# Kernel optimization log

Measured on AMD Instinct MI355X. Metric: run time of the kernel, lower is better.

Reference implementation:

```python
import jax, jax.numpy as jnp
import numpy as np

DIM, PATCHES, HID, NCLS, NBLK, PS = 384, 196, 1536, 1000, 24, 16

def fq(w, bits=8):
    # symmetric per-tensor fake quantization (dequantized), as in QAT DynamicQLinear
    n = float(2 ** (bits - 1) - 1)
    s = jnp.max(jnp.abs(w)) / n + 1e-8
    q = jnp.clip(jnp.round(w / s), -n - 1.0, n) * s
    return q

def setup_inputs() -> dict:
    key = jax.random.key(0)
    ks = jax.random.split(key, 12)
    d = {}
    d["x"] = jax.random.normal(ks[0], (64, 3, 224, 224), jnp.float32)
    d["conv_w"] = jax.random.normal(ks[1], (DIM, 3, PS, PS), jnp.float32) * 0.02
    d["conv_b"] = jnp.zeros((DIM,), jnp.float32)
    d["norm1_a"] = jnp.ones((NBLK, DIM), jnp.float32)
    d["norm1_b"] = jnp.zeros((NBLK, DIM), jnp.float32)
    d["attn_w"] = jax.random.normal(ks[2], (NBLK, PATCHES, PATCHES), jnp.float32) * 0.02
    d["attn_b"] = jnp.zeros((NBLK, PATCHES), jnp.float32)
    d["gamma1"] = jnp.full((NBLK, DIM), 1e-4, jnp.float32)
    d["norm2_a"] = jnp.ones((NBLK, DIM), jnp.float32)
    d["norm2_b"] = jnp.zeros((NBLK, DIM), jnp.float32)
    d["mlp_w1"] = jax.random.normal(ks[3], (NBLK, HID, DIM), jnp.float32) * 0.02
    d["mlp_b1"] = jnp.zeros((NBLK, HID), jnp.float32)
    d["mlp_w2"] = jax.random.normal(ks[4], (NBLK, DIM, HID), jnp.float32) * 0.02
    d["mlp_b2"] = jnp.zeros((NBLK, DIM), jnp.float32)
    d["gamma2"] = jnp.full((NBLK, DIM), 1e-4, jnp.float32)
    d["norm_a"] = jnp.ones((DIM,), jnp.float32)
    d["norm_b"] = jnp.zeros((DIM,), jnp.float32)
    d["head_w"] = jax.random.normal(ks[5], (NCLS, DIM), jnp.float32) * 0.02
    d["head_b"] = jnp.zeros((NCLS,), jnp.float32)
    return d

def reference(x, conv_w, conv_b, norm1_a, norm1_b, attn_w, attn_b, gamma1,
              norm2_a, norm2_b, mlp_w1, mlp_b1, mlp_w2, mlp_b2, gamma2,
              norm_a, norm_b, head_w, head_b):
    B = x.shape[0]
    # patch embed: quantized 16x16 stride-16 conv, then flatten(2).transpose(1,2)
    h = jax.lax.conv_general_dilated(x, fq(conv_w), (PS, PS), 'VALID',
                                     dimension_numbers=('NCHW', 'OIHW', 'NCHW'))
    h = h + conv_b[None, :, None, None]
    h = h.reshape(B, DIM, PATCHES).transpose(0, 2, 1)  # [B, 196, 384]

    def step(xc, p):
        a1, b1, aw, ab, g1, a2, b2, w1, bb1, w2, bb2, g2 = p
        # affine norm1 (per-channel)
        t = xc * a1 + b1
        # cross-patch linear applied on transposed layout: out[b,q,d] = sum_p t[b,p,d] W[q,p]
        t = jnp.einsum('bpd,qp->bqd', t, fq(aw)) + ab[None, :, None]
        xc = g1 * t + xc
        # affine norm2 + MLP (384 -> 1536 -> 384, exact GELU)
        t = xc * a2 + b2
        t = jax.nn.gelu(jnp.einsum('bpd,hd->bph', t, fq(w1)) + bb1, approximate=False)
        t = jnp.einsum('bph,dh->bpd', t, fq(w2)) + bb2
        xc = g2 * t + xc
        return xc, None

    h, _ = jax.lax.scan(step, h, (norm1_a, norm1_b, attn_w, attn_b, gamma1,
                                  norm2_a, norm2_b, mlp_w1, mlp_b1, mlp_w2, mlp_b2, gamma2))
    h = h * norm_a + norm_b          # final affine norm
    h = h.mean(axis=1)               # mean pool over patches -> [B, 384]
    return h @ fq(head_w).T + head_b  # [B, 1000]
```

## Files before the change

kernel.cpp:

```cpp
#include <hip/hip_runtime.h>

#define DIM 384
#define PATCHES 196
#define HID 1536
#define NBLK 24
#define NPAD 256
#define XROWS (64 * PATCHES)
#define BDCOLS (64 * DIM)
#define XELEMS (XROWS * DIM)
#define ESTRIDE 132

typedef __attribute__((ext_vector_type(8))) short s8v;
typedef __attribute__((ext_vector_type(4))) float f4v;
typedef unsigned char uchar;
typedef long long i64t;

__device__ __forceinline__ short f2bf(float f) {
  unsigned u = __float_as_uint(f);
  u += 0x7FFFu + ((u >> 16) & 1u);
  return (short)(u >> 16);
}

__device__ __forceinline__ float gelu_f(float x) {
  float u2 = 1.5957691216f * (x + 0.044715f * x * x * x);
  return x / (1.0f + __expf(-u2));
}

__device__ __forceinline__ unsigned pk4_fp8(float a, float b, float c, float d) {
  int lo = __builtin_amdgcn_cvt_pk_fp8_f32(a, b, 0, false);
  int full = __builtin_amdgcn_cvt_pk_fp8_f32(c, d, lo, true);
  return (unsigned)full;
}
__device__ __forceinline__ uchar fp8_1(float a) {
  return (uchar)(__builtin_amdgcn_cvt_pk_fp8_f32(a, a, 0, false) & 0xff);
}

__device__ __forceinline__ void gload_lds16(const void* g, void* l) {
  __builtin_amdgcn_global_load_lds((const __attribute__((address_space(1))) void*)g,
                                   (__attribute__((address_space(3))) void*)l, 16, 0, 0);
}

__global__ __launch_bounds__(256)
void absmax_v4(const float* __restrict__ src, int f4per, int blocks_per,
               unsigned* __restrict__ out) {
  int tens = blockIdx.x / blocks_per;
  int sl = blockIdx.x - tens * blocks_per;
  const float4* p = (const float4*)(src + (size_t)tens * f4per * 4);
  float m = 0.f;
  for (int i = sl * 256 + threadIdx.x; i < f4per; i += blocks_per * 256) {
    float4 v = p[i];
    m = fmaxf(m, fmaxf(fmaxf(fabsf(v.x), fabsf(v.y)), fmaxf(fabsf(v.z), fabsf(v.w))));
  }
  __shared__ float red[256];
  red[threadIdx.x] = m;
  __syncthreads();
  for (int s = 128; s > 0; s >>= 1) {
    if ((int)threadIdx.x < s) red[threadIdx.x] = fmaxf(red[threadIdx.x], red[threadIdx.x + s]);
    __syncthreads();
  }
  if (threadIdx.x == 0) atomicMax(out + tens, __float_as_uint(red[0]));
}

__global__ __launch_bounds__(256)
void quant_w(const float* __restrict__ w, short* __restrict__ q,
             const unsigned* __restrict__ sc, int per, int total) {
  int i = blockIdx.x * 256 + threadIdx.x;
  if (i >= total) return;
  int tens = i / per;
  float s = __uint_as_float(sc[tens]) / 127.0f + 1e-8f;
  float v = rintf(w[i] / s);
  v = fminf(fmaxf(v, -128.0f), 127.0f) * s;
  q[i] = f2bf(v);
}

__global__ __launch_bounds__(256)
void quant_fp8(const float* __restrict__ w, unsigned* __restrict__ q,
               const unsigned* __restrict__ sc, int per, int total4) {
  int i = blockIdx.x * 256 + threadIdx.x;
  if (i >= total4) return;
  int e = i << 2;
  int tens = e / per;
  float s = __uint_as_float(sc[tens]) / 127.0f + 1e-8f;
  float4 w4 = *(const float4*)(w + e);
  float a = fminf(fmaxf(rintf(w4.x / s), -128.0f), 127.0f) * s;
  float b = fminf(fmaxf(rintf(w4.y / s), -128.0f), 127.0f) * s;
  float c = fminf(fmaxf(rintf(w4.z / s), -128.0f), 127.0f) * s;
  float d = fminf(fmaxf(rintf(w4.w / s), -128.0f), 127.0f) * s;
  q[i] = pk4_fp8(a, b, c, d);
}

__global__ __launch_bounds__(256)
void quant_attn_fp8(const float* __restrict__ w, unsigned* __restrict__ q,
                    const unsigned* __restrict__ sc) {
  int i = blockIdx.x * 256 + threadIdx.x;
  if (i >= NBLK * PATCHES * NPAD / 4) return;
  int e = i << 2;
  int col = e & (NPAD - 1);
  int rt = e >> 8;
  int row = rt % PATCHES;
  int tens = rt / PATCHES;
  float s = __uint_as_float(sc[tens]) / 127.0f + 1e-8f;
  const float* wr = w + (size_t)tens * PATCHES * PATCHES + (size_t)row * PATCHES;
  float v[4];
#pragma unroll
  for (int k = 0; k < 4; ++k) {
    int c = col + k;
    v[k] = (c < PATCHES) ? fminf(fmaxf(rintf(wr[c] / s), -128.0f), 127.0f) * s : 0.f;
  }
  q[i] = pk4_fp8(v[0], v[1], v[2], v[3]);
}

__global__ __launch_bounds__(256)
void quant_head_v4(const float* __restrict__ w, float* __restrict__ q,
                   const unsigned* __restrict__ sc) {
  int i = blockIdx.x * 256 + threadIdx.x;
  if (i >= 1000 * DIM / 4) return;
  float s = __uint_as_float(sc[0]) / 127.0f + 1e-8f;
  float4 w4 = *(const float4*)(w + (i << 2));
  float4 o;
  o.x = fminf(fmaxf(rintf(w4.x / s), -128.0f), 127.0f) * s;
  o.y = fminf(fmaxf(rintf(w4.y / s), -128.0f), 127.0f) * s;
  o.z = fminf(fmaxf(rintf(w4.z / s), -128.0f), 127.0f) * s;
  o.w = fminf(fmaxf(rintf(w4.w / s), -128.0f), 127.0f) * s;
  *(float4*)(q + (i << 2)) = o;
}

__global__ __launch_bounds__(256)
void im2col_k(const float* __restrict__ x, short* __restrict__ Xa) {
  int idx = blockIdx.x * 256 + threadIdx.x;
  if (idx >= XROWS * 768 / 4) return;
  int e = idx << 2;
  int r = e / 768, k = e - r * 768;
  int b = r / PATCHES, p = r - b * PATCHES;
  int c = k >> 8, rem = k & 255, ii = rem >> 4, j = rem & 15;
  int ph = p / 14, pw = p - ph * 14;
  const float4 v = *(const float4*)(x + (b * 3 + c) * 50176 + (ph * 16 + ii) * 224 + pw * 16 + j);
  short2* o = (short2*)(Xa + e);
  o[0] = make_short2(f2bf(v.x), f2bf(v.y));
  o[1] = make_short2(f2bf(v.z), f2bf(v.w));
}

__global__ __launch_bounds__(256)
void gemm_conv(const short* __restrict__ A, const short* __restrict__ B,
               float* __restrict__ Xres, const float* __restrict__ bias,
               const float* __restrict__ n1a, const float* __restrict__ n1b,
               uchar* __restrict__ Yt) {
  constexpr int TILE_SHORTS = 192 * 64;
  __shared__ char smem[2 * TILE_SHORTS * 2];
  short* buf0 = (short*)smem;
  float* S = (float*)smem;
  const int lda = 768, K = 768;

  const int t = threadIdx.x;
  const int lane = t & 63;
  const int wid = t >> 6;
  const int wr = wid >> 1, wc = wid & 1;

  const int gx = gridDim.x;
  const int nwg = gx * gridDim.y;
  const int orig = blockIdx.y * gx + blockIdx.x;
  const int q = nwg >> 3, rm = nwg & 7;
  const int xc = orig & 7, jj = orig >> 3;
  const int wg = (xc < rm ? xc * (q + 1) : rm * (q + 1) + (xc - rm) * q) + jj;
  const int bx = wg % gx, by = wg / gx;
  const int m0 = by * 64, n0 = bx * 128;

  f4v acc[2][4];
#pragma unroll
  for (int m = 0; m < 2; ++m)
#pragma unroll
    for (int n = 0; n < 4; ++n) acc[m][n] = (f4v){0.f, 0.f, 0.f, 0.f};

  const int srow = t >> 3;
  const int scol = ((t & 7) ^ (srow & 7)) << 3;
  const short* ga[2];
#pragma unroll
  for (int h = 0; h < 2; ++h) ga[h] = A + (size_t)(m0 + h * 32 + srow) * lda + scol;
  const short* gb[4];
#pragma unroll
  for (int j = 0; j < 4; ++j) gb[j] = B + (size_t)(n0 + j * 32 + srow) * lda + scol;
  short* ldst = buf0 + (t & ~63) * 8;

  auto stage = [&](int slot, int kt) {
    const int koff = kt << 6;
    const int boff = slot * TILE_SHORTS;
    gload_lds16(ga[0] + koff, ldst + boff);
    gload_lds16(ga[1] + koff, ldst + boff + 2048);
#pragma unroll
    for (int j = 0; j < 4; ++j)
      gload_lds16(gb[j] + koff, ldst + boff + 4096 + j * 2048);
  };

  const int l15 = lane & 15, lk = lane >> 4, l7 = lane & 7;
  int paoff[2], pboff[2];
#pragma unroll
  for (int ks = 0; ks < 2; ++ks) {
    const int cgx = ((ks << 2) + lk) ^ l7;
    paoff[ks] = (wr * 32 + l15) * 64 + (cgx << 3);
    pboff[ks] = 4096 + (wc * 64 + l15) * 64 + (cgx << 3);
  }

  const int nk = K >> 6;
  stage(0, 0);
  asm volatile("s_waitcnt vmcnt(0)" ::: "memory");
  __builtin_amdgcn_s_barrier();
  for (int kt = 0; kt < nk; ++kt) {
    const int cur = kt & 1;
    if (kt + 1 < nk) stage(cur ^ 1, kt + 1);
    const short* base = buf0 + cur * TILE_SHORTS;
    s8v af[2][2], bfr[4][2];
#pragma unroll
    for (int m = 0; m < 2; ++m)
#pragma unroll
      for (int ks = 0; ks < 2; ++ks) af[m][ks] = *(const s8v*)(base + paoff[ks] + m * 1024);
#pragma unroll
    for (int n = 0; n < 4; ++n)
#pragma unroll
      for (int ks = 0; ks < 2; ++ks) bfr[n][ks] = *(const s8v*)(base + pboff[ks] + n * 1024);
    asm volatile("s_waitcnt lgkmcnt(0)" ::: "memory");
    __builtin_amdgcn_sched_barrier(0);
    __builtin_amdgcn_s_setprio(1);
#pragma unroll
    for (int m = 0; m < 2; ++m)
#pragma unroll
      for (int n = 0; n < 4; ++n)
#pragma unroll
        for (int ks = 0; ks < 2; ++ks)
          acc[m][n] = __builtin_amdgcn_mfma_f32_16x16x32_bf16(af[m][ks], bfr[n][ks], acc[m][n], 0, 0, 0);
    __builtin_amdgcn_s_setprio(0);
    if (kt + 1 < nk) {
      asm volatile("s_waitcnt vmcnt(0)" ::: "memory");
      __builtin_amdgcn_s_barrier();
    }
  }

  const int cb = (wc << 6) + l15;
  const int rl = t >> 3;
  const int c0 = (t & 7) << 4;
#pragma unroll
  for (int m = 0; m < 2; ++m) {
    __syncthreads();
#pragma unroll
    for (int n = 0; n < 4; ++n) {
      int c = cb + n * 16;
#pragma unroll
      for (int j = 0; j < 4; ++j)
        S[((wr << 4) + (lk << 2) + j) * ESTRIDE + c] = acc[m][n][j];
    }
    __syncthreads();
    const int r = m0 + (rl >> 4) * 32 + m * 16 + (rl & 15);
    const int colg = n0 + c0;
    float xn[16];
#pragma unroll
    for (int i = 0; i < 4; ++i) {
      float4 q4 = *(const float4*)(S + rl * ESTRIDE + c0 + i * 4);
      float4 b4 = *(const float4*)(bias + colg + i * 4);
      float4 o4 = make_float4(q4.x + b4.x, q4.y + b4.y, q4.z + b4.z, q4.w + b4.w);
      *(float4*)(Xres + (size_t)r * DIM + colg + i * 4) = o4;
      xn[4 * i] = o4.x; xn[4 * i + 1] = o4.y; xn[4 * i + 2] = o4.z; xn[4 * i + 3] = o4.w;
    }
    int bb = r / PATCHES, p = r - bb * PATCHES;
    uchar* yrow = Yt + ((size_t)(bb * DIM + colg)) * NPAD + p;
#pragma unroll
    for (int i = 0; i < 4; ++i) {
      float4 a4 = *(const float4*)(n1a + colg + i * 4);
      float4 b4 = *(const float4*)(n1b + colg + i * 4);
      yrow[(4 * i + 0) * NPAD] = fp8_1(xn[4 * i] * a4.x + b4.x);
      yrow[(4 * i + 1) * NPAD] = fp8_1(xn[4 * i + 1] * a4.y + b4.y);
      yrow[(4 * i + 2) * NPAD] = fp8_1(xn[4 * i + 2] * a4.z + b4.z);
      yrow[(4 * i + 3) * NPAD] = fp8_1(xn[4 * i + 3] * a4.w + b4.w);
    }
  }
}

template <int EPI>
__global__ __launch_bounds__(256)
void gemm8(const uchar* __restrict__ A, int lda8, int Mlim,
           const uchar* __restrict__ B, int ldb8, int K,
           float* __restrict__ Xres, uchar* __restrict__ OutB8,
           const float* __restrict__ bias, const float* __restrict__ gamma,
           const float* __restrict__ n2a, const float* __restrict__ n2b,
           const float* __restrict__ n1a, const float* __restrict__ n1b,
           uchar* __restrict__ Yt) {
  constexpr int TILE_BYTES = 192 * 128;
  __shared__ char smem[2 * TILE_BYTES];
  char* buf0 = smem;
  float* S = (float*)smem;

  const int t = threadIdx.x;
  const int lane = t & 63;
  const int wid = t >> 6;
  const int wr = wid >> 1, wc = wid & 1;

  const int gx = gridDim.x;
  const int nwg = gx * gridDim.y;
  const int orig = blockIdx.y * gx + blockIdx.x;
  const int q = nwg >> 3, rm = nwg & 7;
  const int xc = orig & 7, jj = orig >> 3;
  const int wg = (xc < rm ? xc * (q + 1) : rm * (q + 1) + (xc - rm) * q) + jj;
  const int bx = wg % gx, by = wg / gx;
  const int m0 = by * 64, n0 = bx * 128;

  f4v acc[2][4];
#pragma unroll
  for (int m = 0; m < 2; ++m)
#pragma unroll
    for (int n = 0; n < 4; ++n) acc[m][n] = (f4v){0.f, 0.f, 0.f, 0.f};

  const int srow = t >> 3;
  const int scolB = (((t & 7) ^ (srow & 7)) << 4);
  const uchar* ga[2];
#pragma unroll
  for (int h = 0; h < 2; ++h) {
    int r = m0 + h * 32 + srow;
    if (r >= Mlim) r = Mlim - 1;
    ga[h] = A + (size_t)r * lda8 + scolB;
  }
  const uchar* gb[4];
#pragma unroll
  for (int j = 0; j < 4; ++j)
    gb[j] = B + (size_t)(n0 + j * 32 + srow) * ldb8 + scolB;
  char* ldst = buf0 + (t & ~63) * 16;

  auto stage = [&](int slot, int kt) {
    const int koff = kt << 7;
    const int boff = slot * TILE_BYTES;
    gload_lds16(ga[0] + koff, ldst + boff);
    gload_lds16(ga[1] + koff, ldst + boff + 4096);
#pragma unroll
    for (int j = 0; j < 4; ++j)
      gload_lds16(gb[j] + koff, ldst + boff + 8192 + j * 4096);
  };

  const int l15 = lane & 15, lk = lane >> 4, l7 = lane & 7;
  int cterm[4];
#pragma unroll
  for (int ks = 0; ks < 4; ++ks)
    cterm[ks] = ((((ks << 1) + (lk >> 1)) ^ l7) << 4) + ((lk & 1) << 3);
  int arow[2], brow[4];
#pragma unroll
  for (int m = 0; m < 2; ++m) arow[m] = (wr * 32 + m * 16 + l15) << 7;
#pragma unroll
  for (int n = 0; n < 4; ++n) brow[n] = 8192 + ((wc * 64 + n * 16 + l15) << 7);

  const int nk = K >> 7;
  stage(0, 0);
  asm volatile("s_waitcnt vmcnt(0)" ::: "memory");
  __builtin_amdgcn_s_barrier();
  for (int kt = 0; kt < nk; ++kt) {
    const int cur = kt & 1;
    if (kt + 1 < nk) stage(cur ^ 1, kt + 1);
    const char* base = buf0 + cur * TILE_BYTES;
    i64t af[2][4], bfr[4][4];
#pragma unroll
    for (int m = 0; m < 2; ++m)
#pragma unroll
      for (int ks = 0; ks < 4; ++ks) af[m][ks] = *(const i64t*)(base + arow[m] + cterm[ks]);
#pragma unroll
    for (int n = 0; n < 4; ++n)
#pragma unroll
      for (int ks = 0; ks < 4; ++ks) bfr[n][ks] = *(const i64t*)(base + brow[n] + cterm[ks]);
    asm volatile("s_waitcnt lgkmcnt(0)" ::: "memory");
    __builtin_amdgcn_sched_barrier(0);
    __builtin_amdgcn_s_setprio(1);
#pragma unroll
    for (int ks = 0; ks < 4; ++ks)
#pragma unroll
      for (int m = 0; m < 2; ++m)
#pragma unroll
        for (int n = 0; n < 4; ++n)
          acc[m][n] = __builtin_amdgcn_mfma_f32_16x16x32_fp8_fp8(af[m][ks], bfr[n][ks], acc[m][n], 0, 0, 0);
    __builtin_amdgcn_s_setprio(0);
    if (kt + 1 < nk) {
      asm volatile("s_waitcnt vmcnt(0)" ::: "memory");
      __builtin_amdgcn_s_barrier();
    }
  }

  __syncthreads();
#pragma unroll
  for (int m = 0; m < 2; ++m)
#pragma unroll
    for (int n = 0; n < 4; ++n) {
      int srow2 = wr * 32 + m * 16 + (lk << 2);
      int scol2 = wc * 64 + n * 16 + l15;
#pragma unroll
      for (int j = 0; j < 4; ++j)
        S[(srow2 + j) * ESTRIDE + scol2] = acc[m][n][j];
    }
  __syncthreads();

  if (EPI == 1 || EPI == 2) {
    const int rl = t >> 2;
    const int c0 = (t & 3) << 5;
    const int r = m0 + rl;
    const int colg = n0 + c0;
    float v[32];
#pragma unroll
    for (int i = 0; i < 8; ++i) {
      float4 q4 = *(const float4*)(S + rl * ESTRIDE + c0 + i * 4);
      v[4 * i] = q4.x; v[4 * i + 1] = q4.y; v[4 * i + 2] = q4.z; v[4 * i + 3] = q4.w;
    }
    if (EPI == 1) {
      if (r < Mlim) {
        const int b = colg / DIM, d0 = colg - b * DIM;
        const float br = bias[r];
        const size_t base2 = (size_t)b * (PATCHES * DIM) + (size_t)r * DIM + d0;
        float xn[32];
#pragma unroll
        for (int i = 0; i < 8; ++i) {
          float4 g4 = *(const float4*)(gamma + d0 + i * 4);
          float4 x4 = *(const float4*)(Xres + base2 + i * 4);
          x4.x += g4.x * (v[4 * i] + br);
          x4.y += g4.y * (v[4 * i + 1] + br);
          x4.z += g4.z * (v[4 * i + 2] + br);
          x4.w += g4.w * (v[4 * i + 3] + br);
          *(float4*)(Xres + base2 + i * 4) = x4;
          xn[4 * i] = x4.x; xn[4 * i + 1] = x4.y; xn[4 * i + 2] = x4.z; xn[4 * i + 3] = x4.w;
        }
        unsigned o[8];
#pragma unroll
        for (int i = 0; i < 8; ++i) {
          float4 a4 = *(const float4*)(n2a + d0 + i * 4);
          float4 b4 = *(const float4*)(n2b + d0 + i * 4);
          o[i] = pk4_fp8(xn[4 * i] * a4.x + b4.x, xn[4 * i + 1] * a4.y + b4.y,
                         xn[4 * i + 2] * a4.z + b4.z, xn[4 * i + 3] * a4.w + b4.w);
        }
        *(uint4*)(OutB8 + base2) = make_uint4(o[0], o[1], o[2], o[3]);
        *(uint4*)(OutB8 + base2 + 16) = make_uint4(o[4], o[5], o[6], o[7]);
      }
    } else {
      unsigned o[8];
#pragma unroll
      for (int i = 0; i < 8; ++i) {
        float4 b4 = *(const float4*)(bias + colg + i * 4);
        o[i] = pk4_fp8(gelu_f(v[4 * i] + b4.x), gelu_f(v[4 * i + 1] + b4.y),
                       gelu_f(v[4 * i + 2] + b4.z), gelu_f(v[4 * i + 3] + b4.w));
      }
      uchar* hp = OutB8 + (size_t)r * HID + colg;
      *(uint4*)hp = make_uint4(o[0], o[1], o[2], o[3]);
      *(uint4*)(hp + 16) = make_uint4(o[4], o[5], o[6], o[7]);
    }
  } else {
    const int r0 = m0 + ((t & 15) << 2);
    const int colg = n0 + ((t >> 4) << 3);
    float4 b40 = *(const float4*)(bias + colg);
    float4 b41 = *(const float4*)(bias + colg + 4);
    float4 g40 = *(const float4*)(gamma + colg);
    float4 g41 = *(const float4*)(gamma + colg + 4);
    float xn[4][8];
#pragma unroll
    for (int j = 0; j < 4; ++j) {
      const int rloc = ((t & 15) << 2) + j;
      float4 q0 = *(const float4*)(S + rloc * ESTRIDE + (colg - n0));
      float4 q1 = *(const float4*)(S + rloc * ESTRIDE + (colg - n0) + 4);
      float* xp = Xres + (size_t)(r0 + j) * DIM + colg;
      float4 x0 = *(const float4*)xp;
      float4 x1 = *(const float4*)(xp + 4);
      x0.x += g40.x * (q0.x + b40.x); x0.y += g40.y * (q0.y + b40.y);
      x0.z += g40.z * (q0.z + b40.z); x0.w += g40.w * (q0.w + b40.w);
      x1.x += g41.x * (q1.x + b41.x); x1.y += g41.y * (q1.y + b41.y);
      x1.z += g41.z * (q1.z + b41.z); x1.w += g41.w * (q1.w + b41.w);
      *(float4*)xp = x0;
      *(float4*)(xp + 4) = x1;
      xn[j][0] = x0.x; xn[j][1] = x0.y; xn[j][2] = x0.z; xn[j][3] = x0.w;
      xn[j][4] = x1.x; xn[j][5] = x1.y; xn[j][6] = x1.z; xn[j][7] = x1.w;
    }
    if (Yt != nullptr) {
      const int bb = r0 / PATCHES;
      const int p0 = r0 - bb * PATCHES;
      float a[8], bv[8];
      *(float4*)a = *(const float4*)(n1a + colg);
      *(float4*)(a + 4) = *(const float4*)(n1a + colg + 4);
      *(float4*)bv = *(const float4*)(n1b + colg);
      *(float4*)(bv + 4) = *(const float4*)(n1b + colg + 4);
#pragma unroll
      for (int i = 0; i < 8; ++i) {
        unsigned pk = pk4_fp8(xn[0][i] * a[i] + bv[i], xn[1][i] * a[i] + bv[i],
                              xn[2][i] * a[i] + bv[i], xn[3][i] * a[i] + bv[i]);
        *(unsigned*)(Yt + ((size_t)(bb * DIM + colg + i)) * NPAD + p0) = pk;
      }
    }
  }
}

__global__ __launch_bounds__(256)
void poolnorm2(const float* __restrict__ X, const float* __restrict__ na,
               const float* __restrict__ nb, float* __restrict__ pooled) {
  __shared__ float red[4][64];
  const int b = blockIdx.x, d0 = blockIdx.y * 64;
  const int dl = threadIdx.x & 63, g = threadIdx.x >> 6;
  const float* p = X + (size_t)b * (PATCHES * DIM) + d0 + dl;
  float s = 0.f;
  for (int i = g; i < PATCHES; i += 4) s += p[(size_t)i * DIM];
  red[g][dl] = s;
  __syncthreads();
  if (threadIdx.x < 64) {
    float tot = red[0][dl] + red[1][dl] + red[2][dl] + red[3][dl];
    int d = d0 + dl;
    pooled[b * DIM + d] = (tot * (1.0f / 196.0f)) * na[d] + nb[d];
  }
}

__global__ __launch_bounds__(256)
void head_k2(const float* __restrict__ pooled, const float* __restrict__ Whq,
             const float* __restrict__ hb, float* __restrict__ out) {
  __shared__ float pl[DIM];
  const int b = blockIdx.x, t = threadIdx.x;
  if (t < 192) {
    pl[t] = pooled[b * DIM + t];
    pl[t + 192] = pooled[b * DIM + t + 192];
  }
  __syncthreads();
  const int n = blockIdx.y * 64 + (t >> 2);
  if (n >= 1000) return;
  const int qofs = (t & 3) * 96;
  const float4* w = (const float4*)(Whq + (size_t)n * DIM + qofs);
  const float* p = pl + qofs;
  float s = 0.f;
#pragma unroll 6
  for (int i = 0; i < 24; ++i) {
    float4 wv = w[i];
    s += p[4 * i] * wv.x + p[4 * i + 1] * wv.y + p[4 * i + 2] * wv.z + p[4 * i + 3] * wv.w;
  }
  s += __shfl_down(s, 2, 4);
  s += __shfl_down(s, 1, 4);
  if ((t & 3) == 0) out[b * 1000 + n] = s + hb[n];
}

extern "C" void kernel_launch(void* const* d_in, const int* in_sizes, int n_in,
                              void* d_out, int out_size, void* d_ws, size_t ws_size,
                              hipStream_t stream) {
  const float* x       = (const float*)d_in[0];
  const float* conv_w  = (const float*)d_in[1];
  const float* conv_b  = (const float*)d_in[2];
  const float* norm1_a = (const float*)d_in[3];
  const float* norm1_b = (const float*)d_in[4];
  const float* attn_w  = (const float*)d_in[5];
  const float* attn_b  = (const float*)d_in[6];
  const float* gamma1  = (const float*)d_in[7];
  const float* norm2_a = (const float*)d_in[8];
  const float* norm2_b = (const float*)d_in[9];
  const float* mlp_w1  = (const float*)d_in[10];
  const float* mlp_b1  = (const float*)d_in[11];
  const float* mlp_w2  = (const float*)d_in[12];
  const float* mlp_b2  = (const float*)d_in[13];
  const float* gamma2  = (const float*)d_in[14];
  const float* norm_a  = (const float*)d_in[15];
  const float* norm_b  = (const float*)d_in[16];
  const float* head_w  = (const float*)d_in[17];
  const float* head_b  = (const float*)d_in[18];
  (void)in_sizes; (void)n_in; (void)out_size; (void)ws_size;

  char* ws = (char*)d_ws;
  size_t off = 0;
  auto alloc = [&](size_t bytes) {
    off = (off + 255) & ~(size_t)255;
    void* p = ws + off;
    off += bytes;
    return p;
  };
  unsigned* scales = (unsigned*)alloc(74 * 4);
  short* conv_wq = (short*)alloc((size_t)DIM * 768 * 2);
  uchar* attn_wq = (uchar*)alloc((size_t)NBLK * PATCHES * NPAD);
  uchar* w1q     = (uchar*)alloc((size_t)NBLK * HID * DIM);
  uchar* w2q     = (uchar*)alloc((size_t)NBLK * DIM * HID);
  float* headq   = (float*)alloc((size_t)1000 * DIM * 4);
  float* X       = (float*)alloc((size_t)XELEMS * 4);
  uchar* Yt      = (uchar*)alloc((size_t)BDCOLS * NPAD);
  uchar* Y2      = (uchar*)alloc((size_t)XELEMS);
  uchar* H       = (uchar*)alloc((size_t)XROWS * HID);
  float* pooled  = (float*)alloc((size_t)64 * DIM * 4);
  short* Xa = (short*)H;

  hipMemsetAsync(scales, 0, 74 * 4, stream);
  hipMemsetAsync(Yt, 0, (size_t)BDCOLS * NPAD, stream);
  absmax_v4<<<32, 256, 0, stream>>>(conv_w, DIM * 768 / 4, 32, scales + 0);
  absmax_v4<<<32, 256, 0, stream>>>(head_w, 1000 * DIM / 4, 32, scales + 1);
  absmax_v4<<<NBLK * 8, 256, 0, stream>>>(attn_w, PATCHES * PATCHES / 4, 8, scales + 2);
  absmax_v4<<<NBLK * 64, 256, 0, stream>>>(mlp_w1, HID * DIM / 4, 64, scales + 26);
  absmax_v4<<<NBLK * 64, 256, 0, stream>>>(mlp_w2, DIM * HID / 4, 64, scales + 50);

  quant_w<<<(DIM * 768 + 255) / 256, 256, 0, stream>>>(conv_w, conv_wq, scales + 0, DIM * 768, DIM * 768);
  quant_fp8<<<(NBLK * HID * DIM / 4 + 255) / 256, 256, 0, stream>>>(
      mlp_w1, (unsigned*)w1q, scales + 26, HID * DIM, NBLK * HID * DIM / 4);
  quant_fp8<<<(NBLK * HID * DIM / 4 + 255) / 256, 256, 0, stream>>>(
      mlp_w2, (unsigned*)w2q, scales + 50, DIM * HID, NBLK * DIM * HID / 4);
  quant_attn_fp8<<<(NBLK * PATCHES * NPAD / 4 + 255) / 256, 256, 0, stream>>>(
      attn_w, (unsigned*)attn_wq, scales + 2);
  quant_head_v4<<<(1000 * DIM / 4 + 255) / 256, 256, 0, stream>>>(head_w, headq, scales + 1);

  im2col_k<<<(XROWS * 768 / 4) / 256, 256, 0, stream>>>(x, Xa);
  gemm_conv<<<dim3(3, 196), 256, 0, stream>>>(Xa, conv_wq, X, conv_b, norm1_a, norm1_b, Yt);

  for (int blk = 0; blk < NBLK; ++blk) {
    gemm8<1><<<dim3(BDCOLS / 128, 4), 256, 0, stream>>>(
        attn_wq + (size_t)blk * PATCHES * NPAD, NPAD, PATCHES, Yt, NPAD, NPAD,
        X, Y2, attn_b + blk * PATCHES, gamma1 + blk * DIM,
        norm2_a + blk * DIM, norm2_b + blk * DIM, nullptr, nullptr, nullptr);
    gemm8<2><<<dim3(HID / 128, XROWS / 64), 256, 0, stream>>>(
        Y2, DIM, XROWS, w1q + (size_t)blk * HID * DIM, DIM, DIM,
        nullptr, H, mlp_b1 + blk * HID, nullptr, nullptr, nullptr,
        nullptr, nullptr, nullptr);
    const bool last = (blk == NBLK - 1);
    gemm8<3><<<dim3(DIM / 128, XROWS / 64), 256, 0, stream>>>(
        H, HID, XROWS, w2q + (size_t)blk * DIM * HID, HID, HID,
        X, nullptr, mlp_b2 + blk * DIM, gamma2 + blk * DIM, nullptr, nullptr,
        last ? nullptr : norm1_a + (blk + 1) * DIM,
        last ? nullptr : norm1_b + (blk + 1) * DIM,
        last ? nullptr : Yt);
  }

  poolnorm2<<<dim3(64, 6), 256, 0, stream>>>(X, norm_a, norm_b, pooled);
  head_k2<<<dim3(64, 16), 256, 0, stream>>>(pooled, headq, head_b, (float*)d_out);
}
```

Measured before the change: 2.154 ms.

## Fuse MLP up and down projections into one kernel keeping hidden tile in LDS

Replaces the two separate MLP GEMM launches per block with a single fused kernel. Each workgroup owns 64 token rows and streams W1/W2 chunks of 128 hidden columns. It applies GELU into an fp8 hidden tile held in LDS and accumulates the down projection in registers. This removes the global round trip of the 12544x1536 hidden activation and one launch per block. In exchange it runs only 196 workgroups at occupancy 1 with large LDS use and reloads all weights per workgroup, which may underuse the GPU.

Result: slower. 2.738 ms (+27.1%).

```diff
diff --git a/kernel.cpp b/kernel.cpp
--- a/kernel.cpp
+++ b/kernel.cpp
@@ -273,15 +273,12 @@
   }
 }
 
-template <int EPI>
-__global__ __launch_bounds__(256)
-void gemm8(const uchar* __restrict__ A, int lda8, int Mlim,
-           const uchar* __restrict__ B, int ldb8, int K,
-           float* __restrict__ Xres, uchar* __restrict__ OutB8,
-           const float* __restrict__ bias, const float* __restrict__ gamma,
-           const float* __restrict__ n2a, const float* __restrict__ n2b,
-           const float* __restrict__ n1a, const float* __restrict__ n1b,
-           uchar* __restrict__ Yt) {
+__global__ __launch_bounds__(256)
+void gemm_attn(const uchar* __restrict__ A, int lda8, int Mlim,
+               const uchar* __restrict__ B, int ldb8, int K,
+               float* __restrict__ Xres, uchar* __restrict__ OutB8,
+               const float* __restrict__ bias, const float* __restrict__ gamma,
+               const float* __restrict__ n2a, const float* __restrict__ n2b) {
   constexpr int TILE_BYTES = 192 * 128;
   __shared__ char smem[2 * TILE_BYTES];
   char* buf0 = smem;
@@ -390,95 +387,247 @@
     }
   __syncthreads();
 
-  if (EPI == 1 || EPI == 2) {
-    const int rl = t >> 2;
-    const int c0 = (t & 3) << 5;
-    const int r = m0 + rl;
-    const int colg = n0 + c0;
+  const int rl = t >> 2;
+  const int c0 = (t & 3) << 5;
+  const int r = m0 + rl;
+  const int colg = n0 + c0;
+  if (r < Mlim) {
     float v[32];
 #pragma unroll
     for (int i = 0; i < 8; ++i) {
       float4 q4 = *(const float4*)(S + rl * ESTRIDE + c0 + i * 4);
       v[4 * i] = q4.x; v[4 * i + 1] = q4.y; v[4 * i + 2] = q4.z; v[4 * i + 3] = q4.w;
     }
-    if (EPI == 1) {
-      if (r < Mlim) {
-        const int b = colg / DIM, d0 = colg - b * DIM;
-        const float br = bias[r];
-        const size_t base2 = (size_t)b * (PATCHES * DIM) + (size_t)r * DIM + d0;
-        float xn[32];
-#pragma unroll
-        for (int i = 0; i < 8; ++i) {
-          float4 g4 = *(const float4*)(gamma + d0 + i * 4);
-          float4 x4 = *(const float4*)(Xres + base2 + i * 4);
-          x4.x += g4.x * (v[4 * i] + br);
-          x4.y += g4.y * (v[4 * i + 1] + br);
-          x4.z += g4.z * (v[4 * i + 2] + br);
-          x4.w += g4.w * (v[4 * i + 3] + br);
-          *(float4*)(Xres + base2 + i * 4) = x4;
-          xn[4 * i] = x4.x; xn[4 * i + 1] = x4.y; xn[4 * i + 2] = x4.z; xn[4 * i + 3] = x4.w;
+    const int b = colg / DIM, d0 = colg - b * DIM;
+    const float br = bias[r];
+    const size_t base2 = (size_t)b * (PATCHES * DIM) + (size_t)r * DIM + d0;
+    float xn[32];
+#pragma unroll
+    for (int i = 0; i < 8; ++i) {
+      float4 g4 = *(const float4*)(gamma + d0 + i * 4);
+      float4 x4 = *(const float4*)(Xres + base2 + i * 4);
+      x4.x += g4.x * (v[4 * i] + br);
+      x4.y += g4.y * (v[4 * i + 1] + br);
+      x4.z += g4.z * (v[4 * i + 2] + br);
+      x4.w += g4.w * (v[4 * i + 3] + br);
+      *(float4*)(Xres + base2 + i * 4) = x4;
+      xn[4 * i] = x4.x; xn[4 * i + 1] = x4.y; xn[4 * i + 2] = x4.z; xn[4 * i + 3] = x4.w;
+    }
+    unsigned o[8];
+#pragma unroll
+    for (int i = 0; i < 8; ++i) {
+      float4 a4 = *(const float4*)(n2a + d0 + i * 4);
+      float4 b4 = *(const float4*)(n2b + d0 + i * 4);
+      o[i] = pk4_fp8(xn[4 * i] * a4.x + b4.x, xn[4 * i + 1] * a4.y + b4.y,
+                     xn[4 * i + 2] * a4.z + b4.z, xn[4 * i + 3] * a4.w + b4.w);
+    }
+    *(uint4*)(OutB8 + base2) = make_uint4(o[0], o[1], o[2], o[3]);
+    *(uint4*)(OutB8 + base2 + 16) = make_uint4(o[4], o[5], o[6], o[7]);
+  }
+}
+
+__global__ __launch_bounds__(256, 1)
+void fusedmlp(const uchar* __restrict__ Y2, const uchar* __restrict__ W1,
+              const uchar* __restrict__ W2, float* __restrict__ Xres,
+              const float* __restrict__ b1, const float* __restrict__ b2,
+              const float* __restrict__ g2,
+              const float* __restrict__ n1a, const float* __restrict__ n1b,
+              uchar* __restrict__ Yt) {
+  __shared__ char smem[124416];
+  char* bufW1 = smem;
+  char* bufW2 = smem + 49152;
+  char* Hl    = smem + 98304;
+  float* S    = (float*)(smem + 107520);
+  char* Al    = smem + 98304;
+
+  const int t = threadIdx.x;
+  const int lane = t & 63;
+  const int wid = t >> 6;
+  const int wr = wid >> 1, wc = wid & 1;
+  const int m0 = blockIdx.x * 64;
+  const int l15 = lane & 15, lk = lane >> 4;
+  char* ldwave = (char*)((size_t)(t & ~63) * 16);
+
+  int srow1[12], soff1[12];
+#pragma unroll
+  for (int j = 0; j < 12; ++j) {
+    int idx = j * 256 + t;
+    int row = idx / 24, pos = idx - row * 24;
+    int c = (pos & ~7) | ((pos & 7) ^ (row & 7));
+    srow1[j] = row; soff1[j] = c * 16;
+  }
+
+#pragma unroll
+  for (int j = 0; j < 6; ++j)
+    gload_lds16(Y2 + (size_t)(m0 + srow1[j]) * DIM + soff1[j],
+                Al + j * 4096 + (size_t)ldwave);
+#pragma unroll
+  for (int j = 0; j < 12; ++j)
+    gload_lds16(W1 + (size_t)srow1[j] * DIM + soff1[j],
+                bufW1 + j * 4096 + (size_t)ldwave);
+  asm volatile("s_waitcnt vmcnt(12)" ::: "memory");
+  __builtin_amdgcn_s_barrier();
+
+  i64t af[2][12];
+#pragma unroll
+  for (int m = 0; m < 2; ++m) {
+    const int r = wr * 32 + m * 16 + l15;
+#pragma unroll
+    for (int ks = 0; ks < 12; ++ks) {
+      int c = ks * 2 + (lk >> 1);
+      int pos = (c & ~7) | ((c & 7) ^ (r & 7));
+      af[m][ks] = *(const i64t*)(Al + r * DIM + pos * 16 + (lk & 1) * 8);
+    }
+  }
+
+  f4v acc2[2][12];
+#pragma unroll
+  for (int m = 0; m < 2; ++m)
+#pragma unroll
+    for (int n = 0; n < 12; ++n) acc2[m][n] = (f4v){0.f, 0.f, 0.f, 0.f};
+
+  for (int i = 0; i < 12; ++i) {
+    __syncthreads();
+#pragma unroll
+    for (int j = 0; j < 12; ++j) {
+      int idx = j * 256 + t;
+      int row = idx >> 3;
+      int cc = ((idx & 7) ^ (row & 7)) << 4;
+      gload_lds16(W2 + (size_t)row * HID + i * 128 + cc,
+                  bufW2 + j * 4096 + (size_t)ldwave);
+    }
+    f4v acc1[2][4];
+#pragma unroll
+    for (int m = 0; m < 2; ++m)
+#pragma unroll
+      for (int n = 0; n < 4; ++n) acc1[m][n] = (f4v){0.f, 0.f, 0.f, 0.f};
+#pragma unroll
+    for (int ks = 0; ks < 12; ++ks) {
+      i64t bf[4];
+      const int c = ks * 2 + (lk >> 1);
+#pragma unroll
+      for (int nf = 0; nf < 4; ++nf) {
+        int r = wc * 64 + nf * 16 + l15;
+        int pos = (c & ~7) | ((c & 7) ^ (r & 7));
+        bf[nf] = *(const i64t*)(bufW1 + r * DIM + pos * 16 + (lk & 1) * 8);
+      }
+#pragma unroll
+      for (int m = 0; m < 2; ++m)
+#pragma unroll
+        for (int nf = 0; nf < 4; ++nf)
+          acc1[m][nf] = __builtin_amdgcn_mfma_f32_16x16x32_fp8_fp8(af[m][ks], bf[nf], acc1[m][nf], 0, 0, 0);
+    }
+#pragma unroll
+    for (int hf = 0; hf < 2; ++hf) {
+      __syncthreads();
+      if (wr == hf) {
+#pragma unroll
+        for (int m = 0; m < 2; ++m)
+#pragma unroll
+          for (int nf = 0; nf < 4; ++nf) {
+            int sr = m * 16 + (lk << 2);
+            int scol = wc * 64 + nf * 16 + l15;
+#pragma unroll
+            for (int j = 0; j < 4; ++j)
+              S[(sr + j) * ESTRIDE + scol] = acc1[m][nf][j];
+          }
+      }
+      __syncthreads();
+      {
+        const int rl = t >> 3, c0 = (t & 7) << 4;
+        const int hrow = hf * 32 + rl;
+        unsigned o[4];
+#pragma unroll
+        for (int qq = 0; qq < 4; ++qq) {
+          float4 v4 = *(const float4*)(S + rl * ESTRIDE + c0 + qq * 4);
+          float4 bb = *(const float4*)(b1 + i * 128 + c0 + qq * 4);
+          o[qq] = pk4_fp8(gelu_f(v4.x + bb.x), gelu_f(v4.y + bb.y),
+                          gelu_f(v4.z + bb.z), gelu_f(v4.w + bb.w));
         }
-        unsigned o[8];
-#pragma unroll
-        for (int i = 0; i < 8; ++i) {
-          float4 a4 = *(const float4*)(n2a + d0 + i * 4);
-          float4 b4 = *(const float4*)(n2b + d0 + i * 4);
-          o[i] = pk4_fp8(xn[4 * i] * a4.x + b4.x, xn[4 * i + 1] * a4.y + b4.y,
-                         xn[4 * i + 2] * a4.z + b4.z, xn[4 * i + 3] * a4.w + b4.w);
+        int pos = (t & 7) ^ (hrow & 7);
+        *(uint4*)(Hl + hrow * 128 + pos * 16) = make_uint4(o[0], o[1], o[2], o[3]);
+      }
+    }
+    __syncthreads();
+    if (i + 1 < 12) {
+#pragma unroll
+      for (int j = 0; j < 12; ++j)
+        gload_lds16(W1 + (size_t)((i + 1) * 128 + srow1[j]) * DIM + soff1[j],
+                    bufW1 + j * 4096 + (size_t)ldwave);
+    }
+#pragma unroll
+    for (int ks = 0; ks < 4; ++ks) {
+      const int c = ks * 2 + (lk >> 1);
+      i64t a2[2];
+#pragma unroll
+      for (int m = 0; m < 2; ++m) {
+        int r = wr * 32 + m * 16 + l15;
+        a2[m] = *(const i64t*)(Hl + r * 128 + ((c ^ (r & 7)) << 4) + (lk & 1) * 8);
+      }
+      i64t b2f[12];
+#pragma unroll
+      for (int nf = 0; nf < 12; ++nf) {
+        int r = wc * 192 + nf * 16 + l15;
+        b2f[nf] = *(const i64t*)(bufW2 + r * 128 + ((c ^ (r & 7)) << 4) + (lk & 1) * 8);
+      }
+#pragma unroll
+      for (int m = 0; m < 2; ++m)
+#pragma unroll
+        for (int nf = 0; nf < 12; ++nf)
+          acc2[m][nf] = __builtin_amdgcn_mfma_f32_16x16x32_fp8_fp8(a2[m], b2f[nf], acc2[m][nf], 0, 0, 0);
+    }
+  }
+
+#pragma unroll
+  for (int hf = 0; hf < 2; ++hf) {
+#pragma unroll
+    for (int cb = 0; cb < 3; ++cb) {
+      __syncthreads();
+      if (wr == hf) {
+#pragma unroll
+        for (int m = 0; m < 2; ++m)
+#pragma unroll
+          for (int nf = 0; nf < 12; ++nf) {
+            const int cbase = wc * 192 + nf * 16;
+            if ((cbase >> 7) == cb) {
+              int sr = m * 16 + (lk << 2);
+              int scol = cbase + l15 - cb * 128;
+#pragma unroll
+              for (int j = 0; j < 4; ++j)
+                S[(sr + j) * ESTRIDE + scol] = acc2[m][nf][j];
+            }
+          }
+      }
+      __syncthreads();
+      const int r0 = m0 + hf * 32 + ((t & 7) << 2);
+      const int colg = cb * 128 + ((t >> 3) << 2);
+      float4 b4 = *(const float4*)(b2 + colg);
+      float4 g4 = *(const float4*)(g2 + colg);
+      float xn[4][4];
+#pragma unroll
+      for (int j = 0; j < 4; ++j) {
+        const int rloc = ((t & 7) << 2) + j;
+        float4 q0 = *(const float4*)(S + rloc * ESTRIDE + ((t >> 3) << 2));
+        float* xp = Xres + (size_t)(r0 + j) * DIM + colg;
+        float4 x0 = *(const float4*)xp;
+        x0.x += g4.x * (q0.x + b4.x); x0.y += g4.y * (q0.y + b4.y);
+        x0.z += g4.z * (q0.z + b4.z); x0.w += g4.w * (q0.w + b4.w);
+        *(float4*)xp = x0;
+        xn[j][0] = x0.x; xn[j][1] = x0.y; xn[j][2] = x0.z; xn[j][3] = x0.w;
+      }
+      if (Yt != nullptr) {
+        const int bb = r0 / PATCHES;
+        const int p0 = r0 - bb * PATCHES;
+        float4 a4 = *(const float4*)(n1a + colg);
+        float4 bv4 = *(const float4*)(n1b + colg);
+        float a[4] = {a4.x, a4.y, a4.z, a4.w};
+        float bv[4] = {bv4.x, bv4.y, bv4.z, bv4.w};
+#pragma unroll
+        for (int ii = 0; ii < 4; ++ii) {
+          unsigned pk = pk4_fp8(xn[0][ii] * a[ii] + bv[ii], xn[1][ii] * a[ii] + bv[ii],
+                                xn[2][ii] * a[ii] + bv[ii], xn[3][ii] * a[ii] + bv[ii]);
+          *(unsigned*)(Yt + ((size_t)(bb * DIM + colg + ii)) * NPAD + p0) = pk;
         }
-        *(uint4*)(OutB8 + base2) = make_uint4(o[0], o[1], o[2], o[3]);
-        *(uint4*)(OutB8 + base2 + 16) = make_uint4(o[4], o[5], o[6], o[7]);
-      }
-    } else {
-      unsigned o[8];
-#pragma unroll
-      for (int i = 0; i < 8; ++i) {
-        float4 b4 = *(const float4*)(bias + colg + i * 4);
-        o[i] = pk4_fp8(gelu_f(v[4 * i] + b4.x), gelu_f(v[4 * i + 1] + b4.y),
-                       gelu_f(v[4 * i + 2] + b4.z), gelu_f(v[4 * i + 3] + b4.w));
-      }
-      uchar* hp = OutB8 + (size_t)r * HID + colg;
-      *(uint4*)hp = make_uint4(o[0], o[1], o[2], o[3]);
-      *(uint4*)(hp + 16) = make_uint4(o[4], o[5], o[6], o[7]);
-    }
-  } else {
-    const int r0 = m0 + ((t & 15) << 2);
-    const int colg = n0 + ((t >> 4) << 3);
-    float4 b40 = *(const float4*)(bias + colg);
-    float4 b41 = *(const float4*)(bias + colg + 4);
-    float4 g40 = *(const float4*)(gamma + colg);
-    float4 g41 = *(const float4*)(gamma + colg + 4);
-    float xn[4][8];
-#pragma unroll
-    for (int j = 0; j < 4; ++j) {
-      const int rloc = ((t & 15) << 2) + j;
-      float4 q0 = *(const float4*)(S + rloc * ESTRIDE + (colg - n0));
-      float4 q1 = *(const float4*)(S + rloc * ESTRIDE + (colg - n0) + 4);
-      float* xp = Xres + (size_t)(r0 + j) * DIM + colg;
-      float4 x0 = *(const float4*)xp;
-      float4 x1 = *(const float4*)(xp + 4);
-      x0.x += g40.x * (q0.x + b40.x); x0.y += g40.y * (q0.y + b40.y);
-      x0.z += g40.z * (q0.z + b40.z); x0.w += g40.w * (q0.w + b40.w);
-      x1.x += g41.x * (q1.x + b41.x); x1.y += g41.y * (q1.y + b41.y);
-      x1.z += g41.z * (q1.z + b41.z); x1.w += g41.w * (q1.w + b41.w);
-      *(float4*)xp = x0;
-      *(float4*)(xp + 4) = x1;
-      xn[j][0] = x0.x; xn[j][1] = x0.y; xn[j][2] = x0.z; xn[j][3] = x0.w;
-      xn[j][4] = x1.x; xn[j][5] = x1.y; xn[j][6] = x1.z; xn[j][7] = x1.w;
-    }
-    if (Yt != nullptr) {
-      const int bb = r0 / PATCHES;
-      const int p0 = r0 - bb * PATCHES;
-      float a[8], bv[8];
-      *(float4*)a = *(const float4*)(n1a + colg);
-      *(float4*)(a + 4) = *(const float4*)(n1a + colg + 4);
-      *(float4*)bv = *(const float4*)(n1b + colg);
-      *(float4*)(bv + 4) = *(const float4*)(n1b + colg + 4);
-#pragma unroll
-      for (int i = 0; i < 8; ++i) {
-        unsigned pk = pk4_fp8(xn[0][i] * a[i] + bv[i], xn[1][i] * a[i] + bv[i],
-                              xn[2][i] * a[i] + bv[i], xn[3][i] * a[i] + bv[i]);
-        *(unsigned*)(Yt + ((size_t)(bb * DIM + colg + i)) * NPAD + p0) = pk;
       }
     }
   }
@@ -569,9 +718,8 @@
   float* X       = (float*)alloc((size_t)XELEMS * 4);
   uchar* Yt      = (uchar*)alloc((size_t)BDCOLS * NPAD);
   uchar* Y2      = (uchar*)alloc((size_t)XELEMS);
-  uchar* H       = (uchar*)alloc((size_t)XROWS * HID);
+  short* Xa      = (short*)alloc((size_t)XROWS * 768 * 2);
   float* pooled  = (float*)alloc((size_t)64 * DIM * 4);
-  short* Xa = (short*)H;
 
   hipMemsetAsync(scales, 0, 74 * 4, stream);
   hipMemsetAsync(Yt, 0, (size_t)BDCOLS * NPAD, stream);
@@ -594,18 +742,14 @@
   gemm_conv<<<dim3(3, 196), 256, 0, stream>>>(Xa, conv_wq, X, conv_b, norm1_a, norm1_b, Yt);
 
   for (int blk = 0; blk < NBLK; ++blk) {
-    gemm8<1><<<dim3(BDCOLS / 128, 4), 256, 0, stream>>>(
+    gemm_attn<<<dim3(BDCOLS / 128, 4), 256, 0, stream>>>(
         attn_wq + (size_t)blk * PATCHES * NPAD, NPAD, PATCHES, Yt, NPAD, NPAD,
         X, Y2, attn_b + blk * PATCHES, gamma1 + blk * DIM,
-        norm2_a + blk * DIM, norm2_b + blk * DIM, nullptr, nullptr, nullptr);
-    gemm8<2><<<dim3(HID / 128, XROWS / 64), 256, 0, stream>>>(
-        Y2, DIM, XROWS, w1q + (size_t)blk * HID * DIM, DIM, DIM,
-        nullptr, H, mlp_b1 + blk * HID, nullptr, nullptr, nullptr,
-        nullptr, nullptr, nullptr);
+        norm2_a + blk * DIM, norm2_b + blk * DIM);
     const bool last = (blk == NBLK - 1);
-    gemm8<3><<<dim3(DIM / 128, XROWS / 64), 256, 0, stream>>>(
-        H, HID, XROWS, w2q + (size_t)blk * DIM * HID, HID, HID,
-        X, nullptr, mlp_b2 + blk * DIM, gamma2 + blk * DIM, nullptr, nullptr,
+    fusedmlp<<<196, 256, 0, stream>>>(
+        Y2, w1q + (size_t)blk * HID * DIM, w2q + (size_t)blk * DIM * HID,
+        X, mlp_b1 + blk * HID, mlp_b2 + blk * DIM, gamma2 + blk * DIM,
         last ? nullptr : norm1_a + (blk + 1) * DIM,
         last ? nullptr : norm1_b + (blk + 1) * DIM,
         last ? nullptr : Yt);
```
